# Performance work log

Hardware: AMD Instinct MI355X
Metric: run time of the kernel (lower is better)

The kernel has to match this reference:

```python
import jax, jax.numpy as jnp
import numpy as np
from jax import lax


def setup_inputs() -> dict:
    key = jax.random.key(0)
    k1, k2 = jax.random.split(key)
    N, dim, m = 8192, 1024, 1024
    x = jax.random.normal(k1, (N, dim), dtype=jnp.float32)
    vectors = jax.random.normal(k2, (m, dim), dtype=jnp.float32) * 0.01
    bias = jnp.zeros((dim,), dtype=jnp.float32)
    return {"x": x, "vectors": vectors, "bias": bias}


def reference(x, vectors, bias):
    # Normalize each reflection vector to unit length: [m, d]
    v_normed = vectors / jnp.linalg.norm(vectors, axis=1, keepdims=True)

    def step(out, v):
        # out: [N, d], v: [d]
        proj = out @ v                       # [N]
        out = out - 2.0 * proj[:, None] * v  # rank-1 Householder update
        return out, None

    out, _ = lax.scan(step, x, v_normed)
    return out + bias
```

## Files before the change

kernel.cpp:

```cpp
#include <hip/hip_runtime.h>
#include <hip/hip_bf16.h>

typedef __attribute__((ext_vector_type(8))) short short8;
typedef __attribute__((ext_vector_type(4))) short s16x4;
typedef __attribute__((ext_vector_type(4))) float f32x4;

static __device__ inline short f2bf(float f) {
    unsigned u = __float_as_uint(f);
    unsigned r = (u + 0x7fffu + ((u >> 16) & 1u)) >> 16;
    return (short)r;
}
static __device__ inline float bf2f(short h) {
    return __uint_as_float(((unsigned)(unsigned short)h) << 16);
}

static __device__ inline int swz32(int row, int slot) {
    return row * 32 + ((slot ^ ((row >> 1) & 3)) << 3);
}

__global__ __launch_bounds__(256) void k_norms(const float* __restrict__ vec,
                                               float* __restrict__ inv, int dim) {
    int row = blockIdx.x * 4 + (threadIdx.x >> 6);
    int lane = threadIdx.x & 63;
    const float4* src = (const float4*)(vec + (size_t)row * dim);
    float ss = 0.f;
#pragma unroll
    for (int i = 0; i < 4; ++i) {
        float4 v = src[lane + 64 * i];
        ss += v.x * v.x + v.y * v.y + v.z * v.z + v.w * v.w;
    }
#pragma unroll
    for (int off = 32; off; off >>= 1) ss += __shfl_xor(ss, off, 64);
    if (lane == 0) inv[row] = 1.0f / sqrtf(ss);
}

__global__ __launch_bounds__(256) void k_prep2(const float* __restrict__ vec,
                                               const float* __restrict__ inv,
                                               short* __restrict__ Vh, short* __restrict__ Vl,
                                               short* __restrict__ Vth, short* __restrict__ Vtl,
                                               int m, int dim) {
    __shared__ float tile[32][33];
    int c0 = blockIdx.x * 32, r0 = blockIdx.y * 32;
    int t = threadIdx.x;
    int r = t >> 3, c4 = (t & 7) * 4;
    float iv = inv[r0 + r];
    float4 v = *(const float4*)&vec[(size_t)(r0 + r) * dim + c0 + c4];
    float f[4] = {v.x * iv, v.y * iv, v.z * iv, v.w * iv};
    s16x4 h, l;
#pragma unroll
    for (int q = 0; q < 4; ++q) {
        h[q] = f2bf(f[q]);
        l[q] = f2bf(f[q] - bf2f(h[q]));
        tile[r][c4 + q] = f[q];
    }
    *(s16x4*)&Vh[(size_t)(r0 + r) * dim + c0 + c4] = h;
    *(s16x4*)&Vl[(size_t)(r0 + r) * dim + c0 + c4] = l;
    __syncthreads();
    s16x4 th, tl;
#pragma unroll
    for (int q = 0; q < 4; ++q) {
        float ff = tile[c4 + q][r];
        th[q] = f2bf(ff);
        tl[q] = f2bf(ff - bf2f(th[q]));
    }
    *(s16x4*)&Vth[(size_t)(c0 + r) * m + r0 + c4] = th;
    *(s16x4*)&Vtl[(size_t)(c0 + r) * m + r0 + c4] = tl;
}

__global__ __launch_bounds__(256) void k_cast(const float* __restrict__ X,
                                              short* __restrict__ Xh, int n4) {
    for (int i = blockIdx.x * blockDim.x + threadIdx.x; i < n4; i += gridDim.x * blockDim.x) {
        float4 v = ((const float4*)X)[i];
        float f[4] = {v.x, v.y, v.z, v.w};
        s16x4 h;
#pragma unroll
        for (int q = 0; q < 4; ++q) h[q] = f2bf(f[q]);
        *(s16x4*)&Xh[(size_t)i * 4] = h;
    }
}

template<int MODE, int TRI>
__global__ __launch_bounds__(256) void k_nt64p(
    const short* __restrict__ Ah, const short* __restrict__ Al,
    const short* __restrict__ Bh, const short* __restrict__ Bl,
    float* __restrict__ Cf, short* __restrict__ Ch, short* __restrict__ Cl,
    int K, int lda, int ldb, int ldc) {
    __shared__ short As[2][2][64 * 32];
    __shared__ short Bs[2][2][64 * 32];
    int i0 = blockIdx.y * 64, j0 = blockIdx.x * 64;
    if (TRI == 2 && j0 < i0) return;
    int KE = (TRI == 1) ? (j0 + 64) : K;
    int t = threadIdx.x, lane = t & 63, wave = t >> 6;
    int wr = wave >> 1, wc = wave & 1;
    int srow = t >> 2, slot = t & 3;
    int sofs = swz32(srow, slot);
    int gofs = slot * 8;
    const short* gA_h = &Ah[(size_t)(i0 + srow) * lda + gofs];
    const short* gA_l = &Al[(size_t)(i0 + srow) * lda + gofs];
    const short* gB_h = &Bh[(size_t)(j0 + srow) * ldb + gofs];
    const short* gB_l = &Bl[(size_t)(j0 + srow) * ldb + gofs];
    short8 pAh = *(const short8*)&gA_h[0];
    short8 pAl = *(const short8*)&gA_l[0];
    short8 pBh = *(const short8*)&gB_h[0];
    short8 pBl = *(const short8*)&gB_l[0];
    *(short8*)&As[0][0][sofs] = pAh;
    *(short8*)&As[0][1][sofs] = pAl;
    *(short8*)&Bs[0][0][sofs] = pBh;
    *(short8*)&Bs[0][1][sofs] = pBl;
    f32x4 acc[2][2] = {};
    int nIter = KE >> 5;
    int cur = 0;
    for (int it = 0; it < nIter; ++it) {
        __syncthreads();
        int kn = (it + 1) << 5;
        bool have = kn < KE;
        if (have) {
            pAh = *(const short8*)&gA_h[kn];
            pAl = *(const short8*)&gA_l[kn];
            pBh = *(const short8*)&gB_h[kn];
            pBl = *(const short8*)&gB_l[kn];
        }
        int g = lane >> 4;
        short8 ah[2], al2[2], bh[2], bl2[2];
#pragma unroll
        for (int i = 0; i < 2; ++i) {
            int ro = swz32(wr * 32 + i * 16 + (lane & 15), g);
            ah[i] = *(const short8*)&As[cur][0][ro];
            al2[i] = *(const short8*)&As[cur][1][ro];
        }
#pragma unroll
        for (int j = 0; j < 2; ++j) {
            int ro = swz32(wc * 32 + j * 16 + (lane & 15), g);
            bh[j] = *(const short8*)&Bs[cur][0][ro];
            bl2[j] = *(const short8*)&Bs[cur][1][ro];
        }
#pragma unroll
        for (int i = 0; i < 2; ++i)
#pragma unroll
            for (int j = 0; j < 2; ++j) {
                acc[i][j] = __builtin_amdgcn_mfma_f32_16x16x32_bf16(ah[i], bh[j], acc[i][j], 0, 0, 0);
                acc[i][j] = __builtin_amdgcn_mfma_f32_16x16x32_bf16(ah[i], bl2[j], acc[i][j], 0, 0, 0);
                acc[i][j] = __builtin_amdgcn_mfma_f32_16x16x32_bf16(al2[i], bh[j], acc[i][j], 0, 0, 0);
            }
        if (have) {
            *(short8*)&As[cur ^ 1][0][sofs] = pAh;
            *(short8*)&As[cur ^ 1][1][sofs] = pAl;
            *(short8*)&Bs[cur ^ 1][0][sofs] = pBh;
            *(short8*)&Bs[cur ^ 1][1][sofs] = pBl;
        }
        cur ^= 1;
    }
#pragma unroll
    for (int i = 0; i < 2; ++i)
#pragma unroll
        for (int j = 0; j < 2; ++j) {
            int row0 = i0 + wr * 32 + i * 16 + ((lane >> 4) << 2);
            int col = j0 + wc * 32 + j * 16 + (lane & 15);
#pragma unroll
            for (int r = 0; r < 4; ++r) {
                float v = acc[i][j][r];
                size_t idx = (size_t)(row0 + r) * ldc + col;
                if (MODE == 2) {
                    Ch[idx] = f2bf((((row0 + r) == col) ? 1.f : 0.f) - v);
                } else {
                    short h = f2bf(v);
                    short l = f2bf(v - bf2f(h));
                    Ch[idx] = h;
                    Cl[idx] = l;
                    if (MODE == 3) Cf[idx] = v;
                }
            }
        }
}

__global__ __launch_bounds__(256) void k_baseinv2(const float* __restrict__ G,
                                                  short* __restrict__ Th, short* __restrict__ Tl,
                                                  short* __restrict__ Tth, short* __restrict__ Ttl,
                                                  int m) {
    __shared__ float Rs[64 * 64];
    int d = blockIdx.x >> 4, g = blockIdx.x & 15;
    int b0 = d * 64;
    int t = threadIdx.x, lane = t & 63, wave = t >> 6;
    {
        int r = t >> 2, c00 = (t & 3) * 16;
#pragma unroll
        for (int q = 0; q < 4; ++q)
            *(float4*)&Rs[r * 64 + c00 + q * 4] =
                *(const float4*)&G[(size_t)(b0 + r) * m + b0 + c00 + q * 4];
    }
    __syncthreads();
    int c = g * 4 + wave;
    float x = 0.f;
    for (int r = c; r >= 0; --r) {
        float prod = Rs[r * 64 + lane] * x;
        float s = prod;
#pragma unroll
        for (int off = 32; off; off >>= 1) s += __shfl_xor(s, off, 64);
        if (lane == r) x = ((r == c) ? 2.f : 0.f) - 2.f * s;
    }
    short h = f2bf(x);
    short l = f2bf(x - bf2f(h));
    Th[(size_t)(b0 + lane) * m + b0 + c] = h;
    Tl[(size_t)(b0 + lane) * m + b0 + c] = l;
    Tth[(size_t)(b0 + c) * m + b0 + lane] = h;
    Ttl[(size_t)(b0 + c) * m + b0 + lane] = l;
}

__global__ __launch_bounds__(256) void k_tree64f(const float* __restrict__ G,
                                                 short* __restrict__ Th, short* __restrict__ Tl,
                                                 short* __restrict__ Tth, short* __restrict__ Ttl,
                                                 int m) {
    __shared__ float Gb[64 * 65];
    __shared__ float Ai[64 * 65];
    __shared__ float Ci[64 * 64];
    __shared__ float Tm[64 * 64];
    int p = blockIdx.x;
    int a0 = p * 128, c0 = a0 + 64;
    int t = threadIdx.x;
    {
        int r = t >> 2, c00 = (t & 3) * 16;
#pragma unroll
        for (int q = 0; q < 4; ++q) {
            *(float4*)&Gb[r * 65 + c00 + q * 4] =
                *(const float4*)&G[(size_t)(a0 + r) * m + c0 + c00 + q * 4];
            s16x4 ha = *(const s16x4*)&Th[(size_t)(a0 + r) * m + a0 + c00 + q * 4];
            s16x4 la = *(const s16x4*)&Tl[(size_t)(a0 + r) * m + a0 + c00 + q * 4];
            s16x4 hc = *(const s16x4*)&Th[(size_t)(c0 + r) * m + c0 + c00 + q * 4];
            s16x4 lc = *(const s16x4*)&Tl[(size_t)(c0 + r) * m + c0 + c00 + q * 4];
#pragma unroll
            for (int e = 0; e < 4; ++e) {
                Ai[r * 65 + c00 + q * 4 + e] = bf2f(ha[e]) + bf2f(la[e]);
                Ci[r * 64 + c00 + q * 4 + e] = bf2f(hc[e]) + bf2f(lc[e]);
            }
        }
    }
    __syncthreads();
    int tx = t & 15, ty = t >> 4;
    float acc[4][4] = {};
#pragma unroll 4
    for (int k = 0; k < 64; ++k) {
        float av[4], bv[4];
#pragma unroll
        for (int i = 0; i < 4; ++i) av[i] = Gb[(ty * 4 + i) * 65 + k];
#pragma unroll
        for (int j = 0; j < 4; ++j) bv[j] = Ci[k * 64 + tx * 4 + j];
#pragma unroll
        for (int i = 0; i < 4; ++i)
#pragma unroll
            for (int j = 0; j < 4; ++j) acc[i][j] += av[i] * bv[j];
    }
#pragma unroll
    for (int i = 0; i < 4; ++i)
#pragma unroll
        for (int j = 0; j < 4; ++j) Tm[(ty * 4 + i) * 64 + tx * 4 + j] = acc[i][j];
    __syncthreads();
    float acc2[4][4] = {};
#pragma unroll 4
    for (int k = 0; k < 64; ++k) {
        float av[4], bv[4];
#pragma unroll
        for (int i = 0; i < 4; ++i) av[i] = Ai[(ty * 4 + i) * 65 + k];
#pragma unroll
        for (int j = 0; j < 4; ++j) bv[j] = Tm[k * 64 + tx * 4 + j];
#pragma unroll
        for (int i = 0; i < 4; ++i)
#pragma unroll
            for (int j = 0; j < 4; ++j) acc2[i][j] += av[i] * bv[j];
    }
#pragma unroll
    for (int i = 0; i < 4; ++i)
#pragma unroll
        for (int j = 0; j < 4; ++j) {
            float v = -acc2[i][j];
            short h = f2bf(v);
            short l = f2bf(v - bf2f(h));
            int R = a0 + ty * 4 + i, C = c0 + tx * 4 + j;
            Th[(size_t)R * m + C] = h;
            Tl[(size_t)R * m + C] = l;
            Tth[(size_t)C * m + R] = h;
            Ttl[(size_t)C * m + R] = l;
        }
}

template<int PHASE>
__global__ __launch_bounds__(256) void k_trimm(
    const short* __restrict__ Ah, const short* __restrict__ Al,
    const short* __restrict__ Bh, const short* __restrict__ Bl,
    short* __restrict__ C1h, short* __restrict__ C1l,
    short* __restrict__ C2h, short* __restrict__ C2l,
    int m, int s) {
    __shared__ short As[2][64 * 32];
    __shared__ short Bs[2][64 * 32];
    int p = blockIdx.z;
    int a0 = 2 * p * s, c0 = a0 + s;
    int r0 = blockIdx.y * 64, ct = blockIdx.x * 64;
    int KS = (PHASE == 1) ? 0 : r0;
    int KE = (PHASE == 1) ? (ct + 64) : s;
    size_t tbase = (size_t)p * s * s;
    int t = threadIdx.x, lane = t & 63, wave = t >> 6;
    int wr = wave >> 1, wc = wave & 1;
    int srow = t >> 2, slot = t & 3;
    int sofs = swz32(srow, slot);
    int gofs = slot * 8;
    f32x4 acc[2][2] = {};
    for (int k0 = KS; k0 < KE; k0 += 32) {
        __syncthreads();
        if (PHASE == 1) {
            *(short8*)&As[0][sofs] = *(const short8*)&Ah[(size_t)(a0 + r0 + srow) * m + c0 + k0 + gofs];
            *(short8*)&As[1][sofs] = *(const short8*)&Al[(size_t)(a0 + r0 + srow) * m + c0 + k0 + gofs];
            *(short8*)&Bs[0][sofs] = *(const short8*)&Bh[(size_t)(c0 + ct + srow) * m + c0 + k0 + gofs];
            *(short8*)&Bs[1][sofs] = *(const short8*)&Bl[(size_t)(c0 + ct + srow) * m + c0 + k0 + gofs];
        } else {
            *(short8*)&As[0][sofs] = *(const short8*)&Ah[(size_t)(a0 + r0 + srow) * m + a0 + k0 + gofs];
            *(short8*)&As[1][sofs] = *(const short8*)&Al[(size_t)(a0 + r0 + srow) * m + a0 + k0 + gofs];
            *(short8*)&Bs[0][sofs] = *(const short8*)&Bh[tbase + (size_t)(ct + srow) * s + k0 + gofs];
            *(short8*)&Bs[1][sofs] = *(const short8*)&Bl[tbase + (size_t)(ct + srow) * s + k0 + gofs];
        }
        __syncthreads();
        int g = lane >> 4;
        short8 ah[2], al2[2], bh[2], bl2[2];
#pragma unroll
        for (int i = 0; i < 2; ++i) {
            int ro = swz32(wr * 32 + i * 16 + (lane & 15), g);
            ah[i] = *(const short8*)&As[0][ro];
            al2[i] = *(const short8*)&As[1][ro];
        }
#pragma unroll
        for (int j = 0; j < 2; ++j) {
            int ro = swz32(wc * 32 + j * 16 + (lane & 15), g);
            bh[j] = *(const short8*)&Bs[0][ro];
            bl2[j] = *(const short8*)&Bs[1][ro];
        }
#pragma unroll
        for (int i = 0; i < 2; ++i)
#pragma unroll
            for (int j = 0; j < 2; ++j) {
                acc[i][j] = __builtin_amdgcn_mfma_f32_16x16x32_bf16(ah[i], bh[j], acc[i][j], 0, 0, 0);
                acc[i][j] = __builtin_amdgcn_mfma_f32_16x16x32_bf16(ah[i], bl2[j], acc[i][j], 0, 0, 0);
                acc[i][j] = __builtin_amdgcn_mfma_f32_16x16x32_bf16(al2[i], bh[j], acc[i][j], 0, 0, 0);
            }
    }
#pragma unroll
    for (int i = 0; i < 2; ++i)
#pragma unroll
        for (int j = 0; j < 2; ++j) {
            int row0 = r0 + wr * 32 + i * 16 + ((lane >> 4) << 2);
            int col = ct + wc * 32 + j * 16 + (lane & 15);
#pragma unroll
            for (int r = 0; r < 4; ++r) {
                if (PHASE == 1) {
                    float v = acc[i][j][r];
                    short h = f2bf(v);
                    short l = f2bf(v - bf2f(h));
                    size_t idx = tbase + (size_t)col * s + row0 + r;
                    C1h[idx] = h;
                    C1l[idx] = l;
                } else {
                    float v = -acc[i][j][r];
                    short h = f2bf(v);
                    short l = f2bf(v - bf2f(h));
                    int R = a0 + row0 + r, Cc = c0 + col;
                    C1h[(size_t)R * m + Cc] = h;
                    C1l[(size_t)R * m + Cc] = l;
                    C2h[(size_t)Cc * m + R] = h;
                    C2l[(size_t)Cc * m + R] = l;
                }
            }
        }
}

__global__ __launch_bounds__(256) void k_apply5(const short* __restrict__ xh,
                                                const short* __restrict__ Qt,
                                                const float* __restrict__ bias,
                                                float* __restrict__ out, int dim) {
    __shared__ short As[2][128 * 32];
    __shared__ short Bs[2][128 * 32];
    int nwg = gridDim.x * gridDim.y;
    int flat = blockIdx.y * gridDim.x + blockIdx.x;
    int cpx = nwg >> 3;
    int L = (flat & 7) * cpx + (flat >> 3);
    int m0 = (L / gridDim.x) * 128, n0 = (L % gridDim.x) * 128;
    int t = threadIdx.x, lane = t & 63, wave = t >> 6;
    int wr = wave >> 1, wc = wave & 1;
    int srIn = lane >> 2;
    int sslot = (lane & 3) ^ ((lane >> 3) & 3);
    auto stage = [&](int buf, int k0) {
#pragma unroll
        for (int q = 0; q < 2; ++q) {
            int rg = wave * 2 + q;
            int row = rg * 16 + srIn;
            const short* gA = &xh[(size_t)(m0 + row) * dim + k0 + sslot * 8];
            const short* gB = &Qt[(size_t)(n0 + row) * dim + k0 + sslot * 8];
            __builtin_amdgcn_global_load_lds(
                (const __attribute__((address_space(1))) void*)gA,
                (__attribute__((address_space(3))) void*)&As[buf][rg * 16 * 32], 16, 0, 0);
            __builtin_amdgcn_global_load_lds(
                (const __attribute__((address_space(1))) void*)gB,
                (__attribute__((address_space(3))) void*)&Bs[buf][rg * 16 * 32], 16, 0, 0);
        }
    };
    int nIter = dim >> 5;
    stage(0, 0);
    f32x4 acc[4][4] = {};
    for (int it = 0; it < nIter; ++it) {
        int c = it & 1;
        if (it + 1 < nIter) {
            stage(c ^ 1, (it + 1) << 5);
            asm volatile("s_waitcnt vmcnt(4)" ::: "memory");
        } else {
            asm volatile("s_waitcnt vmcnt(0)" ::: "memory");
        }
        __builtin_amdgcn_s_barrier();
        __builtin_amdgcn_sched_barrier(0);
        int g = lane >> 4;
        short8 af[4], bf_[4];
#pragma unroll
        for (int i = 0; i < 4; ++i)
            af[i] = *(const short8*)&As[c][swz32(wr * 64 + i * 16 + (lane & 15), g)];
#pragma unroll
        for (int j = 0; j < 4; ++j)
            bf_[j] = *(const short8*)&Bs[c][swz32(wc * 64 + j * 16 + (lane & 15), g)];
#pragma unroll
        for (int i = 0; i < 4; ++i)
#pragma unroll
            for (int j = 0; j < 4; ++j)
                acc[i][j] = __builtin_amdgcn_mfma_f32_16x16x32_bf16(af[i], bf_[j], acc[i][j], 0, 0, 0);
        asm volatile("s_waitcnt lgkmcnt(0)" ::: "memory");
        __builtin_amdgcn_s_barrier();
    }
#pragma unroll
    for (int i = 0; i < 4; ++i)
#pragma unroll
        for (int j = 0; j < 4; ++j) {
            int row = m0 + wr * 64 + i * 16 + (lane >> 4) * 4;
            int col = n0 + wc * 64 + j * 16 + (lane & 15);
            float b = bias[col];
#pragma unroll
            for (int r = 0; r < 4; ++r)
                out[(size_t)(row + r) * dim + col] = acc[i][j][r] + b;
        }
}

extern "C" void kernel_launch(void* const* d_in, const int* in_sizes, int n_in,
                              void* d_out, int out_size, void* d_ws, size_t ws_size,
                              hipStream_t stream) {
    const float* x = (const float*)d_in[0];
    const float* vec = (const float*)d_in[1];
    const float* bias = (const float*)d_in[2];
    float* out = (float*)d_out;

    int dim = in_sizes[2];
    int m = in_sizes[1] / dim;
    int n = in_sizes[0] / dim;

    const size_t MD = (size_t)m * dim;
    const size_t MM = (size_t)m * m;

    char* cur = (char*)d_ws;
    auto alloc_f = [&](size_t nelem) { float* p = (float*)cur; cur += nelem * 4; return p; };
    auto alloc_s = [&](size_t nelem) { short* p = (short*)cur; cur += nelem * 2; return p; };
    float* G    = alloc_f(MM);
    float* invn = alloc_f(m);
    short* Vh  = alloc_s(MD);
    short* Vl  = alloc_s(MD);
    short* Vth = alloc_s(MD);
    short* Vtl = alloc_s(MD);
    short* Gh  = alloc_s(MM);
    short* Gl  = alloc_s(MM);
    short* Th  = alloc_s(MM);
    short* Tl  = alloc_s(MM);
    short* Tth = alloc_s(MM);
    short* Ttl = alloc_s(MM);
    short* Wh  = alloc_s(MD);
    short* Wl  = alloc_s(MD);
    short* Qt  = alloc_s((size_t)dim * dim);
    short* tmph = alloc_s(MM / 2);
    short* tmpl = alloc_s(MM / 2);
    short* xh  = alloc_s((size_t)n * dim);

    k_norms<<<m / 4, 256, 0, stream>>>(vec, invn, dim);
    k_prep2<<<dim3(dim / 32, m / 32), 256, 0, stream>>>(vec, invn, Vh, Vl, Vth, Vtl, m, dim);

    k_nt64p<3, 2><<<dim3(m / 64, m / 64), 256, 0, stream>>>(Vh, Vl, Vh, Vl, G, Gh, Gl,
                                                            dim, dim, dim, m);
    k_baseinv2<<<(m / 64) * 16, 256, 0, stream>>>(G, Th, Tl, Tth, Ttl, m);
    k_tree64f<<<m / 128, 256, 0, stream>>>(G, Th, Tl, Tth, Ttl, m);
    for (int s = 128; s < m; s <<= 1) {
        dim3 g(s / 64, s / 64, m / (2 * s));
        k_trimm<1><<<g, 256, 0, stream>>>(Gh, Gl, Tth, Ttl, tmph, tmpl, nullptr, nullptr, m, s);
        k_trimm<2><<<g, 256, 0, stream>>>(Th, Tl, tmph, tmpl, Th, Tl, Tth, Ttl, m, s);
    }

    k_nt64p<1, 1><<<dim3(m / 64, dim / 64), 256, 0, stream>>>(Vth, Vtl, Tth, Ttl, nullptr, Wh, Wl,
                                                              m, m, m, m);
    k_nt64p<2, 0><<<dim3(dim / 64, dim / 64), 256, 0, stream>>>(Vth, Vtl, Wh, Wl, nullptr, Qt, nullptr,
                                                                m, m, m, dim);

    k_cast<<<2048, 256, 0, stream>>>(x, xh, (int)((size_t)n * dim / 4));
    k_apply5<<<dim3(dim / 128, n / 128), 256, 0, stream>>>(xh, Qt, bias, out, dim);
}
```

Baseline: 171.8 us.

## Fuse x cast into Gram GEMM launch and use single-buffered BK=64 apply GEMM

Removes the standalone fp32-to-bf16 cast kernel and runs the cast in 512 extra workgroups appended to the triangular Gram GEMM grid, so it overlaps with that small-grid kernel. It also rewrites the final apply GEMM to stage 64-wide K tiles with a new 8-slot XOR swizzle and plain __syncthreads, replacing the double-buffered 32-wide pipeline. This halves the number of K iterations and barriers but gives up overlap of global loads with MFMA work. The Gram GEMM now uses a flat 1D grid index.

```diff
diff --git a/kernel.cpp b/kernel.cpp
--- a/kernel.cpp
+++ b/kernel.cpp
@@ -16,6 +16,9 @@
 
 static __device__ inline int swz32(int row, int slot) {
     return row * 32 + ((slot ^ ((row >> 1) & 3)) << 3);
+}
+static __device__ inline int swz64(int row, int slot) {
+    return row * 64 + ((slot ^ (row & 7)) << 3);
 }
 
 __global__ __launch_bounds__(256) void k_norms(const float* __restrict__ vec,
@@ -67,27 +70,30 @@
     *(s16x4*)&Vtl[(size_t)(c0 + r) * m + r0 + c4] = tl;
 }
 
-__global__ __launch_bounds__(256) void k_cast(const float* __restrict__ X,
-                                              short* __restrict__ Xh, int n4) {
-    for (int i = blockIdx.x * blockDim.x + threadIdx.x; i < n4; i += gridDim.x * blockDim.x) {
-        float4 v = ((const float4*)X)[i];
-        float f[4] = {v.x, v.y, v.z, v.w};
-        s16x4 h;
-#pragma unroll
-        for (int q = 0; q < 4; ++q) h[q] = f2bf(f[q]);
-        *(s16x4*)&Xh[(size_t)i * 4] = h;
-    }
-}
-
 template<int MODE, int TRI>
-__global__ __launch_bounds__(256) void k_nt64p(
+__global__ __launch_bounds__(256) void k_nt64pc(
     const short* __restrict__ Ah, const short* __restrict__ Al,
     const short* __restrict__ Bh, const short* __restrict__ Bl,
     float* __restrict__ Cf, short* __restrict__ Ch, short* __restrict__ Cl,
-    int K, int lda, int ldb, int ldc) {
+    int K, int lda, int ldb, int ldc, int gw, int nTiles,
+    const float* __restrict__ castX, short* __restrict__ castXh, int castN4) {
     __shared__ short As[2][2][64 * 32];
     __shared__ short Bs[2][2][64 * 32];
-    int i0 = blockIdx.y * 64, j0 = blockIdx.x * 64;
+    int flat = blockIdx.x;
+    if (flat >= nTiles) {
+        int idx = (flat - nTiles) * 256 + threadIdx.x;
+        int stride = (gridDim.x - nTiles) * 256;
+        for (int i = idx; i < castN4; i += stride) {
+            float4 v = ((const float4*)castX)[i];
+            float f[4] = {v.x, v.y, v.z, v.w};
+            s16x4 h;
+#pragma unroll
+            for (int q = 0; q < 4; ++q) h[q] = f2bf(f[q]);
+            *(s16x4*)&castXh[(size_t)i * 4] = h;
+        }
+        return;
+    }
+    int i0 = (flat / gw) * 64, j0 = (flat % gw) * 64;
     if (TRI == 2 && j0 < i0) return;
     int KE = (TRI == 1) ? (j0 + 64) : K;
     int t = threadIdx.x, lane = t & 63, wave = t >> 6;
@@ -369,12 +375,12 @@
         }
 }
 
-__global__ __launch_bounds__(256) void k_apply5(const short* __restrict__ xh,
+__global__ __launch_bounds__(256) void k_apply3(const short* __restrict__ xh,
                                                 const short* __restrict__ Qt,
                                                 const float* __restrict__ bias,
                                                 float* __restrict__ out, int dim) {
-    __shared__ short As[2][128 * 32];
-    __shared__ short Bs[2][128 * 32];
+    __shared__ short As[128 * 64];
+    __shared__ short Bs[128 * 64];
     int nwg = gridDim.x * gridDim.y;
     int flat = blockIdx.y * gridDim.x + blockIdx.x;
     int cpx = nwg >> 3;
@@ -382,51 +388,41 @@
     int m0 = (L / gridDim.x) * 128, n0 = (L % gridDim.x) * 128;
     int t = threadIdx.x, lane = t & 63, wave = t >> 6;
     int wr = wave >> 1, wc = wave & 1;
-    int srIn = lane >> 2;
-    int sslot = (lane & 3) ^ ((lane >> 3) & 3);
-    auto stage = [&](int buf, int k0) {
-#pragma unroll
-        for (int q = 0; q < 2; ++q) {
-            int rg = wave * 2 + q;
-            int row = rg * 16 + srIn;
+    int sr = lane >> 3;
+    int sslot = (lane & 7) ^ (sr & 7);
+    f32x4 acc[4][4] = {};
+    for (int k0 = 0; k0 < dim; k0 += 64) {
+        __syncthreads();
+#pragma unroll
+        for (int q = 0; q < 4; ++q) {
+            int rg = wave * 4 + q;
+            int row = rg * 8 + sr;
             const short* gA = &xh[(size_t)(m0 + row) * dim + k0 + sslot * 8];
             const short* gB = &Qt[(size_t)(n0 + row) * dim + k0 + sslot * 8];
             __builtin_amdgcn_global_load_lds(
                 (const __attribute__((address_space(1))) void*)gA,
-                (__attribute__((address_space(3))) void*)&As[buf][rg * 16 * 32], 16, 0, 0);
+                (__attribute__((address_space(3))) void*)&As[rg * 8 * 64], 16, 0, 0);
             __builtin_amdgcn_global_load_lds(
                 (const __attribute__((address_space(1))) void*)gB,
-                (__attribute__((address_space(3))) void*)&Bs[buf][rg * 16 * 32], 16, 0, 0);
-        }
-    };
-    int nIter = dim >> 5;
-    stage(0, 0);
-    f32x4 acc[4][4] = {};
-    for (int it = 0; it < nIter; ++it) {
-        int c = it & 1;
-        if (it + 1 < nIter) {
-            stage(c ^ 1, (it + 1) << 5);
-            asm volatile("s_waitcnt vmcnt(4)" ::: "memory");
-        } else {
-            asm volatile("s_waitcnt vmcnt(0)" ::: "memory");
-        }
-        __builtin_amdgcn_s_barrier();
-        __builtin_amdgcn_sched_barrier(0);
-        int g = lane >> 4;
-        short8 af[4], bf_[4];
-#pragma unroll
-        for (int i = 0; i < 4; ++i)
-            af[i] = *(const short8*)&As[c][swz32(wr * 64 + i * 16 + (lane & 15), g)];
-#pragma unroll
-        for (int j = 0; j < 4; ++j)
-            bf_[j] = *(const short8*)&Bs[c][swz32(wc * 64 + j * 16 + (lane & 15), g)];
-#pragma unroll
-        for (int i = 0; i < 4; ++i)
+                (__attribute__((address_space(3))) void*)&Bs[rg * 8 * 64], 16, 0, 0);
+        }
+        __syncthreads();
+#pragma unroll
+        for (int kk = 0; kk < 2; ++kk) {
+            int g = kk * 4 + (lane >> 4);
+            short8 af[4], bf_[4];
+#pragma unroll
+            for (int i = 0; i < 4; ++i)
+                af[i] = *(const short8*)&As[swz64(wr * 64 + i * 16 + (lane & 15), g)];
 #pragma unroll
             for (int j = 0; j < 4; ++j)
-                acc[i][j] = __builtin_amdgcn_mfma_f32_16x16x32_bf16(af[i], bf_[j], acc[i][j], 0, 0, 0);
-        asm volatile("s_waitcnt lgkmcnt(0)" ::: "memory");
-        __builtin_amdgcn_s_barrier();
+                bf_[j] = *(const short8*)&Bs[swz64(wc * 64 + j * 16 + (lane & 15), g)];
+#pragma unroll
+            for (int i = 0; i < 4; ++i)
+#pragma unroll
+                for (int j = 0; j < 4; ++j)
+                    acc[i][j] = __builtin_amdgcn_mfma_f32_16x16x32_bf16(af[i], bf_[j], acc[i][j], 0, 0, 0);
+        }
     }
 #pragma unroll
     for (int i = 0; i < 4; ++i)
@@ -478,11 +474,16 @@
     short* tmpl = alloc_s(MM / 2);
     short* xh  = alloc_s((size_t)n * dim);
 
+    int gw = m / 64;
+    int nTiles = gw * gw;
+    int castN4 = (int)((size_t)n * dim / 4);
+
     k_norms<<<m / 4, 256, 0, stream>>>(vec, invn, dim);
     k_prep2<<<dim3(dim / 32, m / 32), 256, 0, stream>>>(vec, invn, Vh, Vl, Vth, Vtl, m, dim);
 
-    k_nt64p<3, 2><<<dim3(m / 64, m / 64), 256, 0, stream>>>(Vh, Vl, Vh, Vl, G, Gh, Gl,
-                                                            dim, dim, dim, m);
+    k_nt64pc<3, 2><<<nTiles + 512, 256, 0, stream>>>(Vh, Vl, Vh, Vl, G, Gh, Gl,
+                                                     dim, dim, dim, m, gw, nTiles,
+                                                     x, xh, castN4);
     k_baseinv2<<<(m / 64) * 16, 256, 0, stream>>>(G, Th, Tl, Tth, Ttl, m);
     k_tree64f<<<m / 128, 256, 0, stream>>>(G, Th, Tl, Tth, Ttl, m);
     for (int s = 128; s < m; s <<= 1) {
@@ -491,11 +492,12 @@
         k_trimm<2><<<g, 256, 0, stream>>>(Th, Tl, tmph, tmpl, Th, Tl, Tth, Ttl, m, s);
     }
 
-    k_nt64p<1, 1><<<dim3(m / 64, dim / 64), 256, 0, stream>>>(Vth, Vtl, Tth, Ttl, nullptr, Wh, Wl,
-                                                              m, m, m, m);
-    k_nt64p<2, 0><<<dim3(dim / 64, dim / 64), 256, 0, stream>>>(Vth, Vtl, Wh, Wl, nullptr, Qt, nullptr,
-                                                                m, m, m, dim);
-
-    k_cast<<<2048, 256, 0, stream>>>(x, xh, (int)((size_t)n * dim / 4));
-    k_apply5<<<dim3(dim / 128, n / 128), 256, 0, stream>>>(xh, Qt, bias, out, dim);
-}
+    k_nt64pc<1, 1><<<(m / 64) * (dim / 64), 256, 0, stream>>>(Vth, Vtl, Tth, Ttl, nullptr, Wh, Wl,
+                                                              m, m, m, m, m / 64, (m / 64) * (dim / 64),
+                                                              nullptr, nullptr, 0);
+    k_nt64pc<2, 0><<<(dim / 64) * (dim / 64), 256, 0, stream>>>(Vth, Vtl, Wh, Wl, nullptr, Qt, nullptr,
+                                                                m, m, m, dim, dim / 64, (dim / 64) * (dim / 64),
+                                                                nullptr, nullptr, 0);
+
+    k_apply3<<<dim3(dim / 128, n / 128), 256, 0, stream>>>(xh, Qt, bias, out, dim);
+}
```

Measured after the change: 164.4 us. -4.3%, faster.
